# Kernel optimization log

Hardware: AMD Instinct MI355X
Metric: run time of the kernel (lower is better)

## Reference

```python
import jax, jax.numpy as jnp
import numpy as np

EMBED = 1024
HEADS = 16
HEAD_DIM = EMBED // HEADS


def setup_inputs() -> dict:
    key = jax.random.key(0)
    ks = jax.random.split(key, 11)
    B, S, E = 2, 2048, EMBED
    s = 0.02
    return {
        "query": jax.random.normal(ks[0], (B, S, E), jnp.float32),
        "key_": jax.random.normal(ks[1], (B, S, E), jnp.float32),
        "value": jax.random.normal(ks[2], (B, S, E), jnp.float32),
        "Wq": jax.random.normal(ks[3], (E, E), jnp.float32) * s,
        "bq": jnp.zeros((E,), jnp.float32),
        "Wk": jax.random.normal(ks[4], (E, E), jnp.float32) * s,
        "bk": jnp.zeros((E,), jnp.float32),
        "Wv": jax.random.normal(ks[5], (E, E), jnp.float32) * s,
        "bv": jnp.zeros((E,), jnp.float32),
        "Wo": jax.random.normal(ks[6], (E, E), jnp.float32) * s,
        "bo": jnp.zeros((E,), jnp.float32),
    }


def reference(query, key_, value, Wq, bq, Wk, bk, Wv, bv, Wo, bo):
    B, S, E = query.shape
    H, D = HEADS, HEAD_DIM
    # torch Linear: x @ W.T + b, weight stored [out, in]
    Q = (query @ Wq.T + bq).reshape(B, S, H, D).transpose(0, 2, 1, 3)   # [B,H,S,D]
    K = (key_ @ Wk.T + bk).reshape(B, -1, H, D).transpose(0, 2, 1, 3)
    V = (value @ Wv.T + bv).reshape(B, -1, H, D).transpose(0, 2, 1, 3)
    scores = jnp.einsum("bhsd,bhtd->bhst", Q, K) / jnp.sqrt(jnp.float32(D))
    attn_weights = jax.nn.softmax(scores, axis=-1)                      # dropout p=0.0
    attn_out = jnp.einsum("bhst,bhtd->bhsd", attn_weights, V)
    attn_out = attn_out.transpose(0, 2, 1, 3).reshape(B, S, E)
    output = attn_out @ Wo.T + bo
    return output, attn_weights
```

## Files before the change

kernel.cpp:

```cpp
#include <hip/hip_runtime.h>
#include <hip/hip_bf16.h>
#include <cstdint>
#include <cstddef>

#define Bdim 2
#define Sdim 2048
#define Edim 1024
#define Hdim 16
#define Ddim 64
#define KVB 128
#define MROWS (Bdim*Sdim)

typedef __bf16 bf16_t;
typedef __attribute__((ext_vector_type(8))) __bf16 bf16x8;
typedef __attribute__((ext_vector_type(4))) __bf16 bf16x4;
typedef __attribute__((ext_vector_type(4))) float f32x4;

typedef __attribute__((address_space(3))) uint8_t lds8_t;
typedef const __attribute__((address_space(1))) uint8_t glb8_t;

__device__ inline bf16_t f2b(float x) {
    unsigned u = __builtin_bit_cast(unsigned, x);
    unsigned r = u + 0x7fffu + ((u >> 16) & 1u);
    return __builtin_bit_cast(bf16_t, (unsigned short)(r >> 16));
}

__device__ inline void gemm_async(const bf16_t* A, const bf16_t* B, int K,
                                  f32x4 (&acc)[4][4]) {
    __shared__ __align__(16) bf16_t As[128 * 32];
    __shared__ __align__(16) bf16_t Bs[128 * 32];
    const int tid = threadIdx.x;
    const int lane = tid & 63;
    const int w = tid >> 6;
    const int wm = w >> 1, wn = w & 1;
    const int lr = lane & 15, lg = lane >> 4;

    #pragma unroll
    for (int mi = 0; mi < 4; ++mi)
        #pragma unroll
        for (int ni = 0; ni < 4; ++ni)
            acc[mi][ni] = (f32x4){0.f, 0.f, 0.f, 0.f};

    const int srow = (lane >> 2);
    const int scol = (lane & 3) * 8;

    for (int kt = 0; kt < K; kt += 32) {
        __syncthreads();
        #pragma unroll
        for (int i = 0; i < 2; ++i) {
            const int chunk = w * 2 + i;
            const int row = chunk * 16 + srow;
            __builtin_amdgcn_global_load_lds(
                (glb8_t*)(A + (size_t)row * K + kt + scol),
                (lds8_t*)(As + chunk * 512), 16, 0, 0);
            __builtin_amdgcn_global_load_lds(
                (glb8_t*)(B + (size_t)row * K + kt + scol),
                (lds8_t*)(Bs + chunk * 512), 16, 0, 0);
        }
        __syncthreads();
        bf16x8 af[4], bf[4];
        #pragma unroll
        for (int mi = 0; mi < 4; ++mi)
            af[mi] = *(const bf16x8*)&As[(wm * 64 + mi * 16 + lr) * 32 + lg * 8];
        #pragma unroll
        for (int ni = 0; ni < 4; ++ni)
            bf[ni] = *(const bf16x8*)&Bs[(wn * 64 + ni * 16 + lr) * 32 + lg * 8];
        #pragma unroll
        for (int mi = 0; mi < 4; ++mi)
            #pragma unroll
            for (int ni = 0; ni < 4; ++ni)
                acc[mi][ni] = __builtin_amdgcn_mfma_f32_16x16x32_bf16(
                    af[mi], bf[ni], acc[mi][ni], 0, 0, 0);
    }
}

__global__ __launch_bounds__(256) void k_convert(
    const float* __restrict__ Wq, const float* __restrict__ Wk,
    const float* __restrict__ Wv, const float* __restrict__ Wo,
    const float* __restrict__ xq, const float* __restrict__ xk,
    const float* __restrict__ xv,
    bf16_t* __restrict__ Wb, bf16_t* __restrict__ Xb) {
    const int z = blockIdx.y;
    const float* src;
    bf16_t* d;
    float scale = 1.0f;
    if (z < 4) {
        if (blockIdx.x >= 512) return;
        src = (z == 0) ? Wq : (z == 1) ? Wk : (z == 2) ? Wv : Wo;
        scale = (z == 0) ? 0.125f : 1.0f;
        d = Wb + (size_t)z * Edim * Edim;
    } else {
        src = (z == 4) ? xq : (z == 5) ? xk : xv;
        d = Xb + (size_t)(z - 4) * MROWS * Edim;
    }
    const size_t i = (size_t)blockIdx.x * 256 + threadIdx.x;
    const float4* s4 = (const float4*)(src + i * 8);
    float4 a = s4[0], b = s4[1];
    bf16x8 v;
    v[0] = f2b(a.x * scale); v[1] = f2b(a.y * scale);
    v[2] = f2b(a.z * scale); v[3] = f2b(a.w * scale);
    v[4] = f2b(b.x * scale); v[5] = f2b(b.y * scale);
    v[6] = f2b(b.z * scale); v[7] = f2b(b.w * scale);
    *(bf16x8*)(d + i * 8) = v;
}

__global__ __launch_bounds__(256) void k_proj(
    const bf16_t* __restrict__ Xb, const bf16_t* __restrict__ Wb,
    const float* __restrict__ bq, const float* __restrict__ bk, const float* __restrict__ bv,
    bf16_t* __restrict__ Qb, bf16_t* __restrict__ Kswz, bf16_t* __restrict__ Vswz) {
    const int z = blockIdx.z;
    const bf16_t* X = Xb + (size_t)z * MROWS * Edim;
    const bf16_t* W = Wb + (size_t)z * Edim * Edim;
    const float* bias = (z == 0) ? bq : (z == 1) ? bk : bv;
    const float bscale = (z == 0) ? 0.125f : 1.0f;
    const int tm = blockIdx.y, tn = blockIdx.x;
    f32x4 acc[4][4];
    gemm_async(X + (size_t)tm * 128 * Edim, W + (size_t)tn * 128 * Edim, Edim, acc);
    const int tid = threadIdx.x, lane = tid & 63, w = tid >> 6;
    const int wm = w >> 1, wn = w & 1, lr = lane & 15, lg = lane >> 4;
    #pragma unroll
    for (int mi = 0; mi < 4; ++mi)
        #pragma unroll
        for (int ni = 0; ni < 4; ++ni)
            #pragma unroll
            for (int j = 0; j < 4; ++j) {
                int gm = tm * 128 + wm * 64 + mi * 16 + lg * 4 + j;
                int gn = tn * 128 + wn * 64 + ni * 16 + lr;
                float v = acc[mi][ni][j] + bias[gn] * bscale;
                int b = gm >> 11, s = gm & (Sdim - 1);
                int h = gn >> 6, d = gn & (Ddim - 1);
                size_t bh = (size_t)(b * Hdim + h);
                if (z == 0) {
                    Qb[(bh * Sdim + s) * Ddim + d] = f2b(v);
                } else if (z == 1) {
                    size_t idx = ((bh * (Sdim / 16) + (s >> 4)) * 8 + (d >> 3)) * 128
                               + (s & 15) * 8 + (d & 7);
                    Kswz[idx] = f2b(v);
                } else {
                    size_t idx = (((bh * (Sdim / 32) + (s >> 5)) * 4 + (d >> 4)) * 4
                               + ((s >> 3) & 3)) * 128 + (d & 15) * 8 + (s & 7);
                    Vswz[idx] = f2b(v);
                }
            }
}

__global__ __launch_bounds__(256) void k_attn(
    const bf16_t* __restrict__ Qb, const bf16_t* __restrict__ Kswz,
    const bf16_t* __restrict__ Vswz, float* __restrict__ P, bf16_t* __restrict__ AOb) {
    const int wg = blockIdx.x;
    const int id = ((wg & 7) << 7) | (wg >> 3);
    const int bh = id >> 5, qt = id & 31;
    const int b = bh >> 4, h = bh & 15;
    const int tid = threadIdx.x, lane = tid & 63, w = tid >> 6;
    const int lr = lane & 15, lg = lane >> 4;

    __shared__ bf16_t Ps[2][4][16][132];
    __shared__ float sum_lds[4][64];

    const bf16_t* Qp0 = Qb + ((size_t)bh * Sdim + qt * 64) * Ddim;
    const bf16_t* Qp  = Qp0 + (size_t)(w * 16) * Ddim;
    const bf16_t* Kp = Kswz + (size_t)bh * Sdim * Ddim;
    const bf16_t* Vp = Vswz + (size_t)bh * Ddim * Sdim;
    float* Pp = P + (size_t)bh * Sdim * Sdim + (size_t)(qt * 64 + w * 16) * Sdim;

    {
        bf16x8 qf1[4][2];
        #pragma unroll
        for (int rg = 0; rg < 4; ++rg)
            #pragma unroll
            for (int kk = 0; kk < 2; ++kk)
                qf1[rg][kk] = *(const bf16x8*)(Qp0 + (rg * 16 + lr) * Ddim + kk * 32 + lg * 8);

        float lsum[4][4];
        #pragma unroll
        for (int rg = 0; rg < 4; ++rg)
            #pragma unroll
            for (int j = 0; j < 4; ++j) lsum[rg][j] = 0.f;

        const bf16_t* Kw = Kp + (size_t)w * 32 * 1024;
        bf16x8 bA[2][2], bB[2][2], bC[2][2];
#define LOADG(buf, g) { \
            _Pragma("unroll") \
            for (int t = 0; t < 2; ++t) { \
                const bf16_t* kp = Kw + (size_t)((g) * 2 + t) * 1024 + lane * 8; \
                buf[t][0] = *(const bf16x8*)(kp); \
                buf[t][1] = *(const bf16x8*)(kp + 512); \
            } }
#define COMPG(buf) { \
            f32x4 sv[2][4]; \
            __builtin_amdgcn_s_setprio(1); \
            _Pragma("unroll") \
            for (int t = 0; t < 2; ++t) \
                _Pragma("unroll") \
                for (int rg = 0; rg < 4; ++rg) { \
                    f32x4 s = (f32x4){0.f, 0.f, 0.f, 0.f}; \
                    s = __builtin_amdgcn_mfma_f32_16x16x32_bf16(qf1[rg][0], buf[t][0], s, 0, 0, 0); \
                    s = __builtin_amdgcn_mfma_f32_16x16x32_bf16(qf1[rg][1], buf[t][1], s, 0, 0, 0); \
                    sv[t][rg] = s; \
                } \
            __builtin_amdgcn_s_setprio(0); \
            _Pragma("unroll") \
            for (int t = 0; t < 2; ++t) \
                _Pragma("unroll") \
                for (int rg = 0; rg < 4; ++rg) \
                    _Pragma("unroll") \
                    for (int j = 0; j < 4; ++j) \
                        lsum[rg][j] += __expf(sv[t][rg][j]); }
        LOADG(bA, 0); LOADG(bB, 1);
        for (int g = 0; g < 12; g += 3) {
            LOADG(bC, g + 2); COMPG(bA);
            LOADG(bA, g + 3); COMPG(bB);
            LOADG(bB, g + 4); COMPG(bC);
        }
        LOADG(bC, 14); COMPG(bA);
        LOADG(bA, 15); COMPG(bB);
        COMPG(bC); COMPG(bA);
#undef LOADG
#undef COMPG
        #pragma unroll
        for (int mask = 1; mask <= 8; mask <<= 1)
            #pragma unroll
            for (int rg = 0; rg < 4; ++rg)
                #pragma unroll
                for (int j = 0; j < 4; ++j)
                    lsum[rg][j] += __shfl_xor(lsum[rg][j], mask);
        if (lr == 0)
            #pragma unroll
            for (int rg = 0; rg < 4; ++rg)
                #pragma unroll
                for (int j = 0; j < 4; ++j)
                    sum_lds[w][rg * 16 + lg * 4 + j] = lsum[rg][j];
    }
    __syncthreads();
    float il[4];
    #pragma unroll
    for (int j = 0; j < 4; ++j) {
        int row = w * 16 + lg * 4 + j;
        il[j] = 1.0f / (sum_lds[0][row] + sum_lds[1][row] +
                        sum_lds[2][row] + sum_lds[3][row]);
    }

    bf16x8 qf[2];
    #pragma unroll
    for (int kk = 0; kk < 2; ++kk)
        qf[kk] = *(const bf16x8*)(Qp + lr * Ddim + kk * 32 + lg * 8);

    f32x4 oacc[4];
    #pragma unroll
    for (int nd = 0; nd < 4; ++nd) oacc[nd] = (f32x4){0.f, 0.f, 0.f, 0.f};

    for (int kt = 0; kt < Sdim / KVB; ++kt) {
        const int cur = kt & 1, prev = cur ^ 1;
        bf16x8 kf[8][2];
        #pragma unroll
        for (int ni = 0; ni < 8; ++ni) {
            const bf16_t* kp = Kp + (size_t)(kt * 8 + ni) * 1024 + lane * 8;
            kf[ni][0] = *(const bf16x8*)(kp);
            kf[ni][1] = *(const bf16x8*)(kp + 512);
        }
        bf16x8 vf[4][4];
        #pragma unroll
        for (int ks = 0; ks < 4; ++ks)
            #pragma unroll
            for (int nd = 0; nd < 4; ++nd)
                vf[ks][nd] = *(const bf16x8*)(Vp + ((size_t)(kt * 4 + ks) * 4 + nd) * 512 + lane * 8);
        if (kt > 0) {
            #pragma unroll
            for (int i = 0; i < 8; ++i) {
                int row = 2 * i + (lane >> 5);
                int col0 = (lane & 31) * 4;
                bf16x4 p4 = *(const bf16x4*)&Ps[prev][w][row][col0];
                f32x4 o;
                o[0] = (float)p4[0]; o[1] = (float)p4[1];
                o[2] = (float)p4[2]; o[3] = (float)p4[3];
                *(f32x4*)&Pp[(size_t)row * Sdim + (kt - 1) * KVB + col0] = o;
            }
        }
        __builtin_amdgcn_s_setprio(1);
        #pragma unroll
        for (int ni = 0; ni < 8; ++ni) {
            f32x4 s = (f32x4){0.f, 0.f, 0.f, 0.f};
            s = __builtin_amdgcn_mfma_f32_16x16x32_bf16(qf[0], kf[ni][0], s, 0, 0, 0);
            s = __builtin_amdgcn_mfma_f32_16x16x32_bf16(qf[1], kf[ni][1], s, 0, 0, 0);
            #pragma unroll
            for (int j = 0; j < 4; ++j)
                Ps[cur][w][lg * 4 + j][ni * 16 + lr] = f2b(__expf(s[j]) * il[j]);
        }
        __builtin_amdgcn_s_setprio(0);
        __builtin_amdgcn_s_setprio(1);
        #pragma unroll
        for (int ks = 0; ks < 4; ++ks) {
            bf16x8 pa = *(const bf16x8*)&Ps[cur][w][lr][ks * 32 + lg * 8];
            #pragma unroll
            for (int nd = 0; nd < 4; ++nd)
                oacc[nd] = __builtin_amdgcn_mfma_f32_16x16x32_bf16(pa, vf[ks][nd], oacc[nd], 0, 0, 0);
        }
        __builtin_amdgcn_s_setprio(0);
    }
    #pragma unroll
    for (int i = 0; i < 8; ++i) {
        int row = 2 * i + (lane >> 5);
        int col0 = (lane & 31) * 4;
        bf16x4 p4 = *(const bf16x4*)&Ps[1][w][row][col0];
        f32x4 o;
        o[0] = (float)p4[0]; o[1] = (float)p4[1];
        o[2] = (float)p4[2]; o[3] = (float)p4[3];
        *(f32x4*)&Pp[(size_t)row * Sdim + (Sdim - KVB) + col0] = o;
    }

    #pragma unroll
    for (int nd = 0; nd < 4; ++nd)
        #pragma unroll
        for (int j = 0; j < 4; ++j) {
            int s = qt * 64 + w * 16 + lg * 4 + j;
            int d = nd * 16 + lr;
            AOb[((size_t)(b * Sdim + s)) * Edim + h * Ddim + d] = f2b(oacc[nd][j]);
        }
}

__global__ __launch_bounds__(256) void k_oproj(
    const bf16_t* __restrict__ AOb, const bf16_t* __restrict__ Wob,
    const float* __restrict__ bo, float* __restrict__ out) {
    f32x4 acc[4][4];
    gemm_async(AOb + (size_t)blockIdx.y * 128 * Edim,
               Wob + (size_t)blockIdx.x * 128 * Edim, Edim, acc);
    const int tid = threadIdx.x, lane = tid & 63, w = tid >> 6;
    const int wm = w >> 1, wn = w & 1, lr = lane & 15, lg = lane >> 4;
    #pragma unroll
    for (int mi = 0; mi < 4; ++mi)
        #pragma unroll
        for (int ni = 0; ni < 4; ++ni)
            #pragma unroll
            for (int j = 0; j < 4; ++j) {
                int gm = blockIdx.y * 128 + wm * 64 + mi * 16 + lg * 4 + j;
                int gn = blockIdx.x * 128 + wn * 64 + ni * 16 + lr;
                out[(size_t)gm * Edim + gn] = acc[mi][ni][j] + bo[gn];
            }
}

extern "C" void kernel_launch(void* const* d_in, const int* in_sizes, int n_in,
                              void* d_out, int out_size, void* d_ws, size_t ws_size,
                              hipStream_t stream) {
    const float* query = (const float*)d_in[0];
    const float* key_  = (const float*)d_in[1];
    const float* value = (const float*)d_in[2];
    const float* Wq = (const float*)d_in[3];
    const float* bq = (const float*)d_in[4];
    const float* Wk = (const float*)d_in[5];
    const float* bk = (const float*)d_in[6];
    const float* Wv = (const float*)d_in[7];
    const float* bv = (const float*)d_in[8];
    const float* Wo = (const float*)d_in[9];
    const float* bo = (const float*)d_in[10];

    float* out = (float*)d_out;
    float* P = out + (size_t)MROWS * Edim;
    const size_t PSZ = (size_t)32 * Sdim * Sdim;

    const size_t WSZ = (size_t)Edim * Edim;
    const size_t HSD = (size_t)Bdim * Hdim * Sdim * Ddim;
    bf16_t* Wb   = (bf16_t*)d_ws;
    bf16_t* Qb   = Wb + 4 * WSZ;
    bf16_t* Kswz = Qb + HSD;
    bf16_t* Vswz = Kswz + HSD;
    bf16_t* AOb  = Vswz + HSD;
    bf16_t* Xb   = (bf16_t*)(P + PSZ - 6 * 1024 * 1024);

    k_convert<<<dim3(2048, 7), 256, 0, stream>>>(Wq, Wk, Wv, Wo, query, key_, value,
                                                 Wb, Xb);
    k_proj<<<dim3(8, 32, 3), 256, 0, stream>>>(Xb, Wb, bq, bk, bv, Qb, Kswz, Vswz);
    k_attn<<<dim3(1024), 256, 0, stream>>>(Qb, Kswz, Vswz, P, AOb);
    k_oproj<<<dim3(8, 32, 1), 256, 0, stream>>>(AOb, Wb + 3 * WSZ, bo, out);
}
```

Before: 269.5 us.

## Process two query tiles per attention workgroup, folding tile B's row-sum into tile A's pass

Each attention workgroup now handles two adjacent 64-row query tiles, and the grid is halved. While tile A does its main pass, tile B's softmax denominators are accumulated from the same K fragments already in registers. A second full pass for tile B then writes the probabilities and the output. The aim is to remove the separate row-sum pre-pass for half the tiles, at the cost of fewer workgroups, more register pressure and a serial second pass.

```diff
diff --git a/kernel.cpp b/kernel.cpp
--- a/kernel.cpp
+++ b/kernel.cpp
@@ -148,8 +148,9 @@
     const bf16_t* __restrict__ Qb, const bf16_t* __restrict__ Kswz,
     const bf16_t* __restrict__ Vswz, float* __restrict__ P, bf16_t* __restrict__ AOb) {
     const int wg = blockIdx.x;
-    const int id = ((wg & 7) << 7) | (wg >> 3);
-    const int bh = id >> 5, qt = id & 31;
+    const int id = ((wg & 7) << 6) | (wg >> 3);
+    const int bh = id >> 4, qp = id & 15;
+    const int qtA = qp * 2, qtB = qp * 2 + 1;
     const int b = bh >> 4, h = bh & 15;
     const int tid = threadIdx.x, lane = tid & 63, w = tid >> 6;
     const int lr = lane & 15, lg = lane >> 4;
@@ -157,11 +158,13 @@
     __shared__ bf16_t Ps[2][4][16][132];
     __shared__ float sum_lds[4][64];
 
-    const bf16_t* Qp0 = Qb + ((size_t)bh * Sdim + qt * 64) * Ddim;
-    const bf16_t* Qp  = Qp0 + (size_t)(w * 16) * Ddim;
     const bf16_t* Kp = Kswz + (size_t)bh * Sdim * Ddim;
     const bf16_t* Vp = Vswz + (size_t)bh * Ddim * Sdim;
-    float* Pp = P + (size_t)bh * Sdim * Sdim + (size_t)(qt * 64 + w * 16) * Sdim;
+    const bf16_t* QpA0 = Qb + ((size_t)bh * Sdim + qtA * 64) * Ddim;
+    const bf16_t* QpA  = QpA0 + (size_t)(w * 16) * Ddim;
+    const bf16_t* QpB  = Qb + ((size_t)bh * Sdim + qtB * 64 + w * 16) * Ddim;
+    float* PpA = P + (size_t)bh * Sdim * Sdim + (size_t)(qtA * 64 + w * 16) * Sdim;
+    float* PpB = P + (size_t)bh * Sdim * Sdim + (size_t)(qtB * 64 + w * 16) * Sdim;
 
     {
         bf16x8 qf1[4][2];
@@ -169,7 +172,7 @@
         for (int rg = 0; rg < 4; ++rg)
             #pragma unroll
             for (int kk = 0; kk < 2; ++kk)
-                qf1[rg][kk] = *(const bf16x8*)(Qp0 + (rg * 16 + lr) * Ddim + kk * 32 + lg * 8);
+                qf1[rg][kk] = *(const bf16x8*)(QpA0 + (rg * 16 + lr) * Ddim + kk * 32 + lg * 8);
 
         float lsum[4][4];
         #pragma unroll
@@ -232,22 +235,25 @@
                     sum_lds[w][rg * 16 + lg * 4 + j] = lsum[rg][j];
     }
     __syncthreads();
-    float il[4];
+    float ilA[4];
     #pragma unroll
     for (int j = 0; j < 4; ++j) {
         int row = w * 16 + lg * 4 + j;
-        il[j] = 1.0f / (sum_lds[0][row] + sum_lds[1][row] +
-                        sum_lds[2][row] + sum_lds[3][row]);
-    }
-
-    bf16x8 qf[2];
-    #pragma unroll
-    for (int kk = 0; kk < 2; ++kk)
-        qf[kk] = *(const bf16x8*)(Qp + lr * Ddim + kk * 32 + lg * 8);
+        ilA[j] = 1.0f / (sum_lds[0][row] + sum_lds[1][row] +
+                         sum_lds[2][row] + sum_lds[3][row]);
+    }
+
+    bf16x8 qfA[2], qfB[2];
+    #pragma unroll
+    for (int kk = 0; kk < 2; ++kk) {
+        qfA[kk] = *(const bf16x8*)(QpA + lr * Ddim + kk * 32 + lg * 8);
+        qfB[kk] = *(const bf16x8*)(QpB + lr * Ddim + kk * 32 + lg * 8);
+    }
 
     f32x4 oacc[4];
     #pragma unroll
     for (int nd = 0; nd < 4; ++nd) oacc[nd] = (f32x4){0.f, 0.f, 0.f, 0.f};
+    float lsumB[4] = {0.f, 0.f, 0.f, 0.f};
 
     for (int kt = 0; kt < Sdim / KVB; ++kt) {
         const int cur = kt & 1, prev = cur ^ 1;
@@ -273,20 +279,28 @@
                 f32x4 o;
                 o[0] = (float)p4[0]; o[1] = (float)p4[1];
                 o[2] = (float)p4[2]; o[3] = (float)p4[3];
-                *(f32x4*)&Pp[(size_t)row * Sdim + (kt - 1) * KVB + col0] = o;
+                *(f32x4*)&PpA[(size_t)row * Sdim + (kt - 1) * KVB + col0] = o;
             }
         }
         __builtin_amdgcn_s_setprio(1);
         #pragma unroll
         for (int ni = 0; ni < 8; ++ni) {
             f32x4 s = (f32x4){0.f, 0.f, 0.f, 0.f};
-            s = __builtin_amdgcn_mfma_f32_16x16x32_bf16(qf[0], kf[ni][0], s, 0, 0, 0);
-            s = __builtin_amdgcn_mfma_f32_16x16x32_bf16(qf[1], kf[ni][1], s, 0, 0, 0);
+            s = __builtin_amdgcn_mfma_f32_16x16x32_bf16(qfA[0], kf[ni][0], s, 0, 0, 0);
+            s = __builtin_amdgcn_mfma_f32_16x16x32_bf16(qfA[1], kf[ni][1], s, 0, 0, 0);
             #pragma unroll
             for (int j = 0; j < 4; ++j)
-                Ps[cur][w][lg * 4 + j][ni * 16 + lr] = f2b(__expf(s[j]) * il[j]);
+                Ps[cur][w][lg * 4 + j][ni * 16 + lr] = f2b(__expf(s[j]) * ilA[j]);
         }
         __builtin_amdgcn_s_setprio(0);
+        #pragma unroll
+        for (int ni = 0; ni < 8; ++ni) {
+            f32x4 s = (f32x4){0.f, 0.f, 0.f, 0.f};
+            s = __builtin_amdgcn_mfma_f32_16x16x32_bf16(qfB[0], kf[ni][0], s, 0, 0, 0);
+            s = __builtin_amdgcn_mfma_f32_16x16x32_bf16(qfB[1], kf[ni][1], s, 0, 0, 0);
+            #pragma unroll
+            for (int j = 0; j < 4; ++j) lsumB[j] += __expf(s[j]);
+        }
         __builtin_amdgcn_s_setprio(1);
         #pragma unroll
         for (int ks = 0; ks < 4; ++ks) {
@@ -305,14 +319,92 @@
         f32x4 o;
         o[0] = (float)p4[0]; o[1] = (float)p4[1];
         o[2] = (float)p4[2]; o[3] = (float)p4[3];
-        *(f32x4*)&Pp[(size_t)row * Sdim + (Sdim - KVB) + col0] = o;
-    }
-
+        *(f32x4*)&PpA[(size_t)row * Sdim + (Sdim - KVB) + col0] = o;
+    }
     #pragma unroll
     for (int nd = 0; nd < 4; ++nd)
         #pragma unroll
         for (int j = 0; j < 4; ++j) {
-            int s = qt * 64 + w * 16 + lg * 4 + j;
+            int s = qtA * 64 + w * 16 + lg * 4 + j;
+            int d = nd * 16 + lr;
+            AOb[((size_t)(b * Sdim + s)) * Edim + h * Ddim + d] = f2b(oacc[nd][j]);
+        }
+
+    #pragma unroll
+    for (int mask = 1; mask <= 8; mask <<= 1)
+        #pragma unroll
+        for (int j = 0; j < 4; ++j)
+            lsumB[j] += __shfl_xor(lsumB[j], mask);
+    float ilB[4];
+    #pragma unroll
+    for (int j = 0; j < 4; ++j) ilB[j] = 1.0f / lsumB[j];
+
+    #pragma unroll
+    for (int nd = 0; nd < 4; ++nd) oacc[nd] = (f32x4){0.f, 0.f, 0.f, 0.f};
+
+    for (int kt = 0; kt < Sdim / KVB; ++kt) {
+        const int cur = kt & 1, prev = cur ^ 1;
+        bf16x8 kf[8][2];
+        #pragma unroll
+        for (int ni = 0; ni < 8; ++ni) {
+            const bf16_t* kp = Kp + (size_t)(kt * 8 + ni) * 1024 + lane * 8;
+            kf[ni][0] = *(const bf16x8*)(kp);
+            kf[ni][1] = *(const bf16x8*)(kp + 512);
+        }
+        bf16x8 vf[4][4];
+        #pragma unroll
+        for (int ks = 0; ks < 4; ++ks)
+            #pragma unroll
+            for (int nd = 0; nd < 4; ++nd)
+                vf[ks][nd] = *(const bf16x8*)(Vp + ((size_t)(kt * 4 + ks) * 4 + nd) * 512 + lane * 8);
+        if (kt > 0) {
+            #pragma unroll
+            for (int i = 0; i < 8; ++i) {
+                int row = 2 * i + (lane >> 5);
+                int col0 = (lane & 31) * 4;
+                bf16x4 p4 = *(const bf16x4*)&Ps[prev][w][row][col0];
+                f32x4 o;
+                o[0] = (float)p4[0]; o[1] = (float)p4[1];
+                o[2] = (float)p4[2]; o[3] = (float)p4[3];
+                *(f32x4*)&PpB[(size_t)row * Sdim + (kt - 1) * KVB + col0] = o;
+            }
+        }
+        __builtin_amdgcn_s_setprio(1);
+        #pragma unroll
+        for (int ni = 0; ni < 8; ++ni) {
+            f32x4 s = (f32x4){0.f, 0.f, 0.f, 0.f};
+            s = __builtin_amdgcn_mfma_f32_16x16x32_bf16(qfB[0], kf[ni][0], s, 0, 0, 0);
+            s = __builtin_amdgcn_mfma_f32_16x16x32_bf16(qfB[1], kf[ni][1], s, 0, 0, 0);
+            #pragma unroll
+            for (int j = 0; j < 4; ++j)
+                Ps[cur][w][lg * 4 + j][ni * 16 + lr] = f2b(__expf(s[j]) * ilB[j]);
+        }
+        __builtin_amdgcn_s_setprio(0);
+        __builtin_amdgcn_s_setprio(1);
+        #pragma unroll
+        for (int ks = 0; ks < 4; ++ks) {
+            bf16x8 pa = *(const bf16x8*)&Ps[cur][w][lr][ks * 32 + lg * 8];
+            #pragma unroll
+            for (int nd = 0; nd < 4; ++nd)
+                oacc[nd] = __builtin_amdgcn_mfma_f32_16x16x32_bf16(pa, vf[ks][nd], oacc[nd], 0, 0, 0);
+        }
+        __builtin_amdgcn_s_setprio(0);
+    }
+    #pragma unroll
+    for (int i = 0; i < 8; ++i) {
+        int row = 2 * i + (lane >> 5);
+        int col0 = (lane & 31) * 4;
+        bf16x4 p4 = *(const bf16x4*)&Ps[1][w][row][col0];
+        f32x4 o;
+        o[0] = (float)p4[0]; o[1] = (float)p4[1];
+        o[2] = (float)p4[2]; o[3] = (float)p4[3];
+        *(f32x4*)&PpB[(size_t)row * Sdim + (Sdim - KVB) + col0] = o;
+    }
+    #pragma unroll
+    for (int nd = 0; nd < 4; ++nd)
+        #pragma unroll
+        for (int j = 0; j < 4; ++j) {
+            int s = qtB * 64 + w * 16 + lg * 4 + j;
             int d = nd * 16 + lr;
             AOb[((size_t)(b * Sdim + s)) * Edim + h * Ddim + d] = f2b(oacc[nd][j]);
         }
@@ -369,6 +461,6 @@
     k_convert<<<dim3(2048, 7), 256, 0, stream>>>(Wq, Wk, Wv, Wo, query, key_, value,
                                                  Wb, Xb);
     k_proj<<<dim3(8, 32, 3), 256, 0, stream>>>(Xb, Wb, bq, bk, bv, Qb, Kswz, Vswz);
-    k_attn<<<dim3(1024), 256, 0, stream>>>(Qb, Kswz, Vswz, P, AOb);
+    k_attn<<<dim3(512), 256, 0, stream>>>(Qb, Kswz, Vswz, P, AOb);
     k_oproj<<<dim3(8, 32, 1), 256, 0, stream>>>(AOb, Wb + 3 * WSZ, bo, out);
 }
```

New measurement: 282.4 us. +4.8%, slower.
